# Optimization experiments

Measured on AMD Instinct MI355X. Metric: run time of the kernel, lower is better.

## Reference

```python
import jax, jax.numpy as jnp
import numpy as np
import math

B, H, N, D = 2, 16, 2048, 64

def setup_inputs() -> dict:
    key = jax.random.key(0)
    kq, kk, kv, kb = jax.random.split(key, 4)
    return {
        "query": jax.random.normal(kq, (B, H, N, D), dtype=jnp.float32),
        "key": jax.random.normal(kk, (B, H, N, D), dtype=jnp.float32),
        "value": jax.random.normal(kv, (B, H, N, D), dtype=jnp.float32),
        "relative_position_bias": jax.random.normal(kb, (H, N, N), dtype=jnp.float32),
    }

def reference(query, key, value, relative_position_bias):
    d = query.shape[-1]
    # scores: [B,H,N,N]
    attn = jnp.einsum("bhnd,bhmd->bhnm", query, key) / jnp.sqrt(jnp.asarray(d, query.dtype))
    attn = attn + relative_position_bias[None]  # broadcast over batch
    attn = jax.nn.softmax(attn, axis=-1)
    # dropout p=0.0 -> identity
    output = jnp.einsum("bhnm,bhmd->bhnd", attn, value)
    return (output, attn)
```

## Files before the change

kernel.cpp:

```cpp
#include <hip/hip_runtime.h>
#include <cstdint>

#define BN 2
#define HN 16
#define NN 2048
#define DD 64
#define KT 64
#define NT (NN / KT)
#define LDP 72
#define LDF 68

typedef __attribute__((ext_vector_type(8))) short short8;
typedef __attribute__((ext_vector_type(8))) unsigned short ushort8;
typedef __attribute__((ext_vector_type(4))) float float4v;

static __device__ __forceinline__ unsigned short f2bf(float f){
    uint32_t u = __builtin_bit_cast(uint32_t, f);
    u += 0x7FFFu + ((u >> 16) & 1u);
    return (unsigned short)(u >> 16);
}

static __device__ __forceinline__ float4v mfma_bf16(short8 a, short8 b, float4v c){
    return __builtin_amdgcn_mfma_f32_16x16x32_bf16(a, b, c, 0, 0, 0);
}

static __device__ __forceinline__ void barrier_lds(){
    asm volatile("s_waitcnt lgkmcnt(0)" ::: "memory");
    __builtin_amdgcn_s_barrier();
    asm volatile("" ::: "memory");
}

__launch_bounds__(256, 4)
__global__ void attn_fused_kernel(const float* __restrict__ Q,
                                  const float* __restrict__ K,
                                  const float* __restrict__ V,
                                  const float* __restrict__ Bias,
                                  float* __restrict__ Out){
    __shared__ unsigned short Kb[KT][LDP];
    __shared__ unsigned short Vt[DD][LDP];
    __shared__ float Pb[4][16][LDF];

    const int bid = blockIdx.x;
    const int b   = bid & 1;
    const int t2  = bid >> 1;
    const int rt  = t2 & 31;
    const int h   = t2 >> 5;

    const int tid = threadIdx.x;
    const int l   = tid & 63;
    const int w   = tid >> 6;
    const int lg  = l >> 4;
    const int ll  = l & 15;
    const int vc  = ll * 4;

    const int qw = rt * 64 + w * 16;
    const size_t bh = (size_t)(b * HN + h);
    const float* Qg = Q + (bh * NN + qw) * DD;
    const float* Kg = K + bh * NN * DD;
    const float* Vg = V + bh * NN * DD;
    const float* BgV = Bias + (size_t)h * NN * NN + (size_t)(qw + lg) * NN + vc;

    const int sr = tid >> 2;
    const int sc = (tid & 3) << 4;

    short8 qf[2];
    {
        const float* qrow = Qg + (size_t)ll * DD + lg * 8;
        #pragma unroll
        for(int ks = 0; ks < 2; ++ks){
            float4v f0 = *(const float4v*)(qrow + ks * 32);
            float4v f1 = *(const float4v*)(qrow + ks * 32 + 4);
            short8 s;
            s[0]=(short)f2bf(f0[0]); s[1]=(short)f2bf(f0[1]);
            s[2]=(short)f2bf(f0[2]); s[3]=(short)f2bf(f0[3]);
            s[4]=(short)f2bf(f1[0]); s[5]=(short)f2bf(f1[1]);
            s[6]=(short)f2bf(f1[2]); s[7]=(short)f2bf(f1[3]);
            qf[ks] = s;
        }
    }

    float lsum[4];
    #pragma unroll
    for(int r = 0; r < 4; ++r) lsum[r] = 0.f;

    float4v kreg[4], bv[4];
    {
        const float* src = Kg + (size_t)sr * DD + sc;
        #pragma unroll
        for(int i = 0; i < 4; ++i) kreg[i] = *(const float4v*)(src + i * 4);
        #pragma unroll
        for(int it = 0; it < 4; ++it)
            bv[it] = *(const float4v*)(BgV + (size_t)(it * 4) * NN);
    }

    for(int ct = 0; ct < NT; ++ct){
        barrier_lds();
        {
            unsigned short tmp[16];
            #pragma unroll
            for(int i = 0; i < 4; ++i)
                #pragma unroll
                for(int j = 0; j < 4; ++j)
                    tmp[i*4+j] = f2bf(kreg[i][j]);
            *(ushort8*)&Kb[sr][sc]     = *(ushort8*)&tmp[0];
            *(ushort8*)&Kb[sr][sc + 8] = *(ushort8*)&tmp[8];
        }
        if(ct + 1 < NT){
            const float* src = Kg + (size_t)((ct+1)*KT + sr) * DD + sc;
            #pragma unroll
            for(int i = 0; i < 4; ++i) kreg[i] = *(const float4v*)(src + i * 4);
        }
        barrier_lds();

        #pragma unroll
        for(int it = 0; it < 4; ++it)
            *(float4v*)&Pb[w][it*4 + lg][vc] = bv[it];
        if(ct + 1 < NT){
            #pragma unroll
            for(int it = 0; it < 4; ++it)
                bv[it] = *(const float4v*)(BgV + (size_t)(it * 4) * NN + (ct+1)*KT);
        }

        float4v acc[4];
        #pragma unroll
        for(int sub = 0; sub < 4; ++sub) acc[sub] = (float4v){0.f,0.f,0.f,0.f};
        __builtin_amdgcn_s_setprio(1);
        #pragma unroll
        for(int sub = 0; sub < 4; ++sub){
            short8 b0 = *(const short8*)&Kb[sub*16 + ll][lg*8];
            short8 b1 = *(const short8*)&Kb[sub*16 + ll][32 + lg*8];
            acc[sub] = mfma_bf16(qf[0], b0, acc[sub]);
            acc[sub] = mfma_bf16(qf[1], b1, acc[sub]);
        }
        __builtin_amdgcn_s_setprio(0);

        float e[16];
        #pragma unroll
        for(int sub = 0; sub < 4; ++sub)
            #pragma unroll
            for(int r = 0; r < 4; ++r)
                e[sub*4+r] = __expf(acc[sub][r] * 0.125f + Pb[w][lg*4+r][sub*16+ll]);

        #pragma unroll
        for(int r = 0; r < 4; ++r){
            float ps = (e[r] + e[4+r]) + (e[8+r] + e[12+r]);
            #pragma unroll
            for(int d = 1; d < 16; d <<= 1) ps += __shfl_xor(ps, d);
            lsum[r] += ps;
        }
    }

    float rl[4];
    #pragma unroll
    for(int r = 0; r < 4; ++r) rl[r] = 1.0f / lsum[r];

    float4v oacc[4];
    #pragma unroll
    for(int ds = 0; ds < 4; ++ds) oacc[ds] = (float4v){0.f,0.f,0.f,0.f};

    float* attnW = Out + (size_t)BN*HN*NN*DD
                 + (bh * NN + qw + lg) * (size_t)NN + vc;

    float4v vreg[4];
    {
        const float* ks = Kg + (size_t)sr * DD + sc;
        const float* vs = Vg + (size_t)sr * DD + sc;
        #pragma unroll
        for(int i = 0; i < 4; ++i){
            kreg[i] = *(const float4v*)(ks + i * 4);
            vreg[i] = *(const float4v*)(vs + i * 4);
        }
        #pragma unroll
        for(int it = 0; it < 4; ++it)
            bv[it] = *(const float4v*)(BgV + (size_t)(it * 4) * NN);
    }

    for(int ct = 0; ct < NT; ++ct){
        barrier_lds();
        {
            unsigned short tmp[16];
            #pragma unroll
            for(int i = 0; i < 4; ++i)
                #pragma unroll
                for(int j = 0; j < 4; ++j)
                    tmp[i*4+j] = f2bf(kreg[i][j]);
            *(ushort8*)&Kb[sr][sc]     = *(ushort8*)&tmp[0];
            *(ushort8*)&Kb[sr][sc + 8] = *(ushort8*)&tmp[8];
            #pragma unroll
            for(int i = 0; i < 4; ++i)
                #pragma unroll
                for(int j = 0; j < 4; ++j){
                    const int d = sc + i*4 + j;
                    Vt[d][sr ^ (((d >> 4) & 3) << 4)] = f2bf(vreg[i][j]);
                }
        }
        if(ct + 1 < NT){
            const float* ks = Kg + (size_t)((ct+1)*KT + sr) * DD + sc;
            const float* vs = Vg + (size_t)((ct+1)*KT + sr) * DD + sc;
            #pragma unroll
            for(int i = 0; i < 4; ++i){
                kreg[i] = *(const float4v*)(ks + i * 4);
                vreg[i] = *(const float4v*)(vs + i * 4);
            }
        }
        barrier_lds();

        #pragma unroll
        for(int it = 0; it < 4; ++it)
            *(float4v*)&Pb[w][it*4 + lg][vc] = bv[it];
        if(ct + 1 < NT){
            #pragma unroll
            for(int it = 0; it < 4; ++it)
                bv[it] = *(const float4v*)(BgV + (size_t)(it * 4) * NN + (ct+1)*KT);
        }

        float4v acc[4];
        #pragma unroll
        for(int sub = 0; sub < 4; ++sub) acc[sub] = (float4v){0.f,0.f,0.f,0.f};
        __builtin_amdgcn_s_setprio(1);
        #pragma unroll
        for(int sub = 0; sub < 4; ++sub){
            short8 b0 = *(const short8*)&Kb[sub*16 + ll][lg*8];
            short8 b1 = *(const short8*)&Kb[sub*16 + ll][32 + lg*8];
            acc[sub] = mfma_bf16(qf[0], b0, acc[sub]);
            acc[sub] = mfma_bf16(qf[1], b1, acc[sub]);
        }
        __builtin_amdgcn_s_setprio(0);

        #pragma unroll
        for(int sub = 0; sub < 4; ++sub)
            #pragma unroll
            for(int r = 0; r < 4; ++r){
                float sv = acc[sub][r] * 0.125f + Pb[w][lg*4+r][sub*16+ll];
                Pb[w][lg*4+r][sub*16+ll] = __expf(sv) * rl[r];
            }

        short8 pf0, pf1;
        {
            float4v p0 = *(const float4v*)&Pb[w][ll][lg*8];
            float4v p1 = *(const float4v*)&Pb[w][ll][lg*8 + 4];
            float4v p2 = *(const float4v*)&Pb[w][ll][32 + lg*8];
            float4v p3 = *(const float4v*)&Pb[w][ll][32 + lg*8 + 4];
            #pragma unroll
            for(int j = 0; j < 4; ++j){
                pf0[j]   = (short)f2bf(p0[j]);
                pf0[4+j] = (short)f2bf(p1[j]);
                pf1[j]   = (short)f2bf(p2[j]);
                pf1[4+j] = (short)f2bf(p3[j]);
            }
        }

        #pragma unroll
        for(int it = 0; it < 4; ++it){
            float4v pv = *(const float4v*)&Pb[w][it*4 + lg][vc];
            *(float4v*)(attnW + (size_t)(it*4) * NN + ct*KT) = pv;
        }

        __builtin_amdgcn_s_setprio(1);
        #pragma unroll
        for(int ds = 0; ds < 4; ++ds){
            short8 v0 = *(const short8*)&Vt[ds*16 + ll][(lg*8) ^ (ds<<4)];
            short8 v1 = *(const short8*)&Vt[ds*16 + ll][(32 + lg*8) ^ (ds<<4)];
            oacc[ds] = mfma_bf16(pf0, v0, oacc[ds]);
            oacc[ds] = mfma_bf16(pf1, v1, oacc[ds]);
        }
        __builtin_amdgcn_s_setprio(0);
    }

    float* outG = Out + (bh * NN + qw) * (size_t)DD;
    #pragma unroll
    for(int ds = 0; ds < 4; ++ds)
        #pragma unroll
        for(int r = 0; r < 4; ++r)
            outG[(size_t)(lg*4 + r) * DD + ds*16 + ll] = oacc[ds][r];
}

extern "C" void kernel_launch(void* const* d_in, const int* in_sizes, int n_in,
                              void* d_out, int out_size, void* d_ws, size_t ws_size,
                              hipStream_t stream) {
    const float* q    = (const float*)d_in[0];
    const float* k    = (const float*)d_in[1];
    const float* v    = (const float*)d_in[2];
    const float* bias = (const float*)d_in[3];
    float* out = (float*)d_out;

    dim3 grid(BN * HN * (NN / 64));
    dim3 block(256);
    hipLaunchKernelGGL(attn_fused_kernel, grid, block, 0, stream, q, k, v, bias, out);
}
```

Baseline: 331.0 us.

## Swap MFMA operand order to get transposed score tiles and drop fp32 LDS staging

Swaps the A/B operands of the QK^T and PV MFMAs so each lane holds four consecutive key columns of one query row. Bias can then be loaded straight into registers matching the accumulator layout, and the attention probabilities written to global memory as float4 without the fp32 LDS round-trip. The row-sum reduction shrinks to two cross-lane shuffles after the loop, and P is repacked to bf16 through a small packed LDS buffer for the PV MFMA. Output stores also become vectorized. The cost is extra registers for the double-buffered bias.

```diff
diff --git a/kernel.cpp b/kernel.cpp
--- a/kernel.cpp
+++ b/kernel.cpp
@@ -8,11 +8,12 @@
 #define KT 64
 #define NT (NN / KT)
 #define LDP 72
-#define LDF 68
 
 typedef __attribute__((ext_vector_type(8))) short short8;
 typedef __attribute__((ext_vector_type(8))) unsigned short ushort8;
 typedef __attribute__((ext_vector_type(4))) float float4v;
+typedef __attribute__((ext_vector_type(2))) uint32_t uint2v;
+typedef __attribute__((ext_vector_type(4))) uint32_t uint4v;
 
 static __device__ __forceinline__ unsigned short f2bf(float f){
     uint32_t u = __builtin_bit_cast(uint32_t, f);
@@ -38,7 +39,7 @@
                                   float* __restrict__ Out){
     __shared__ unsigned short Kb[KT][LDP];
     __shared__ unsigned short Vt[DD][LDP];
-    __shared__ float Pb[4][16][LDF];
+    __shared__ __align__(16) uint32_t Pe[4][4][16][12];
 
     const int bid = blockIdx.x;
     const int b   = bid & 1;
@@ -51,14 +52,13 @@
     const int w   = tid >> 6;
     const int lg  = l >> 4;
     const int ll  = l & 15;
-    const int vc  = ll * 4;
 
     const int qw = rt * 64 + w * 16;
     const size_t bh = (size_t)(b * HN + h);
     const float* Qg = Q + (bh * NN + qw) * DD;
     const float* Kg = K + bh * NN * DD;
     const float* Vg = V + bh * NN * DD;
-    const float* BgV = Bias + (size_t)h * NN * NN + (size_t)(qw + lg) * NN + vc;
+    const float* BgA = Bias + (size_t)h * NN * NN + (size_t)(qw + ll) * NN + lg * 4;
 
     const int sr = tid >> 2;
     const int sc = (tid & 3) << 4;
@@ -79,9 +79,7 @@
         }
     }
 
-    float lsum[4];
-    #pragma unroll
-    for(int r = 0; r < 4; ++r) lsum[r] = 0.f;
+    float lsum = 0.f;
 
     float4v kreg[4], bv[4];
     {
@@ -89,8 +87,8 @@
         #pragma unroll
         for(int i = 0; i < 4; ++i) kreg[i] = *(const float4v*)(src + i * 4);
         #pragma unroll
-        for(int it = 0; it < 4; ++it)
-            bv[it] = *(const float4v*)(BgV + (size_t)(it * 4) * NN);
+        for(int sub = 0; sub < 4; ++sub)
+            bv[sub] = *(const float4v*)(BgA + sub * 16);
     }
 
     for(int ct = 0; ct < NT; ++ct){
@@ -112,13 +110,11 @@
         }
         barrier_lds();
 
-        #pragma unroll
-        for(int it = 0; it < 4; ++it)
-            *(float4v*)&Pb[w][it*4 + lg][vc] = bv[it];
-        if(ct + 1 < NT){
-            #pragma unroll
-            for(int it = 0; it < 4; ++it)
-                bv[it] = *(const float4v*)(BgV + (size_t)(it * 4) * NN + (ct+1)*KT);
+        float4v bvN[4];
+        if(ct + 1 < NT){
+            #pragma unroll
+            for(int sub = 0; sub < 4; ++sub)
+                bvN[sub] = *(const float4v*)(BgA + (ct+1)*KT + sub * 16);
         }
 
         float4v acc[4];
@@ -127,39 +123,35 @@
         __builtin_amdgcn_s_setprio(1);
         #pragma unroll
         for(int sub = 0; sub < 4; ++sub){
-            short8 b0 = *(const short8*)&Kb[sub*16 + ll][lg*8];
-            short8 b1 = *(const short8*)&Kb[sub*16 + ll][32 + lg*8];
-            acc[sub] = mfma_bf16(qf[0], b0, acc[sub]);
-            acc[sub] = mfma_bf16(qf[1], b1, acc[sub]);
+            short8 k0 = *(const short8*)&Kb[sub*16 + ll][lg*8];
+            short8 k1 = *(const short8*)&Kb[sub*16 + ll][32 + lg*8];
+            acc[sub] = mfma_bf16(k0, qf[0], acc[sub]);
+            acc[sub] = mfma_bf16(k1, qf[1], acc[sub]);
         }
         __builtin_amdgcn_s_setprio(0);
 
-        float e[16];
         #pragma unroll
         for(int sub = 0; sub < 4; ++sub)
             #pragma unroll
             for(int r = 0; r < 4; ++r)
-                e[sub*4+r] = __expf(acc[sub][r] * 0.125f + Pb[w][lg*4+r][sub*16+ll]);
-
-        #pragma unroll
-        for(int r = 0; r < 4; ++r){
-            float ps = (e[r] + e[4+r]) + (e[8+r] + e[12+r]);
-            #pragma unroll
-            for(int d = 1; d < 16; d <<= 1) ps += __shfl_xor(ps, d);
-            lsum[r] += ps;
-        }
-    }
-
-    float rl[4];
-    #pragma unroll
-    for(int r = 0; r < 4; ++r) rl[r] = 1.0f / lsum[r];
+                lsum += __expf(acc[sub][r] * 0.125f + bv[sub][r]);
+
+        if(ct + 1 < NT){
+            #pragma unroll
+            for(int sub = 0; sub < 4; ++sub) bv[sub] = bvN[sub];
+        }
+    }
+
+    lsum += __shfl_xor(lsum, 16);
+    lsum += __shfl_xor(lsum, 32);
+    const float rl = 1.0f / lsum;
 
     float4v oacc[4];
     #pragma unroll
     for(int ds = 0; ds < 4; ++ds) oacc[ds] = (float4v){0.f,0.f,0.f,0.f};
 
-    float* attnW = Out + (size_t)BN*HN*NN*DD
-                 + (bh * NN + qw + lg) * (size_t)NN + vc;
+    float* attnA = Out + (size_t)BN*HN*NN*DD
+                 + (bh * NN + qw + ll) * (size_t)NN + lg * 4;
 
     float4v vreg[4];
     {
@@ -171,8 +163,8 @@
             vreg[i] = *(const float4v*)(vs + i * 4);
         }
         #pragma unroll
-        for(int it = 0; it < 4; ++it)
-            bv[it] = *(const float4v*)(BgV + (size_t)(it * 4) * NN);
+        for(int sub = 0; sub < 4; ++sub)
+            bv[sub] = *(const float4v*)(BgA + sub * 16);
     }
 
     for(int ct = 0; ct < NT; ++ct){
@@ -205,13 +197,11 @@
         }
         barrier_lds();
 
-        #pragma unroll
-        for(int it = 0; it < 4; ++it)
-            *(float4v*)&Pb[w][it*4 + lg][vc] = bv[it];
-        if(ct + 1 < NT){
-            #pragma unroll
-            for(int it = 0; it < 4; ++it)
-                bv[it] = *(const float4v*)(BgV + (size_t)(it * 4) * NN + (ct+1)*KT);
+        float4v bvN[4];
+        if(ct + 1 < NT){
+            #pragma unroll
+            for(int sub = 0; sub < 4; ++sub)
+                bvN[sub] = *(const float4v*)(BgA + (ct+1)*KT + sub * 16);
         }
 
         float4v acc[4];
@@ -220,40 +210,38 @@
         __builtin_amdgcn_s_setprio(1);
         #pragma unroll
         for(int sub = 0; sub < 4; ++sub){
-            short8 b0 = *(const short8*)&Kb[sub*16 + ll][lg*8];
-            short8 b1 = *(const short8*)&Kb[sub*16 + ll][32 + lg*8];
-            acc[sub] = mfma_bf16(qf[0], b0, acc[sub]);
-            acc[sub] = mfma_bf16(qf[1], b1, acc[sub]);
+            short8 k0 = *(const short8*)&Kb[sub*16 + ll][lg*8];
+            short8 k1 = *(const short8*)&Kb[sub*16 + ll][32 + lg*8];
+            acc[sub] = mfma_bf16(k0, qf[0], acc[sub]);
+            acc[sub] = mfma_bf16(k1, qf[1], acc[sub]);
         }
         __builtin_amdgcn_s_setprio(0);
 
-        #pragma unroll
-        for(int sub = 0; sub < 4; ++sub)
-            #pragma unroll
-            for(int r = 0; r < 4; ++r){
-                float sv = acc[sub][r] * 0.125f + Pb[w][lg*4+r][sub*16+ll];
-                Pb[w][lg*4+r][sub*16+ll] = __expf(sv) * rl[r];
-            }
-
-        short8 pf0, pf1;
-        {
-            float4v p0 = *(const float4v*)&Pb[w][ll][lg*8];
-            float4v p1 = *(const float4v*)&Pb[w][ll][lg*8 + 4];
-            float4v p2 = *(const float4v*)&Pb[w][ll][32 + lg*8];
-            float4v p3 = *(const float4v*)&Pb[w][ll][32 + lg*8 + 4];
-            #pragma unroll
-            for(int j = 0; j < 4; ++j){
-                pf0[j]   = (short)f2bf(p0[j]);
-                pf0[4+j] = (short)f2bf(p1[j]);
-                pf1[j]   = (short)f2bf(p2[j]);
-                pf1[4+j] = (short)f2bf(p3[j]);
-            }
-        }
-
-        #pragma unroll
-        for(int it = 0; it < 4; ++it){
-            float4v pv = *(const float4v*)&Pb[w][it*4 + lg][vc];
-            *(float4v*)(attnW + (size_t)(it*4) * NN + ct*KT) = pv;
+        float4v p4[4];
+        #pragma unroll
+        for(int sub = 0; sub < 4; ++sub)
+            #pragma unroll
+            for(int r = 0; r < 4; ++r)
+                p4[sub][r] = __expf(acc[sub][r] * 0.125f + bv[sub][r]) * rl;
+
+        #pragma unroll
+        for(int sub = 0; sub < 4; ++sub)
+            *(float4v*)(attnA + ct*KT + sub*16) = p4[sub];
+
+        uint32_t pk[8];
+        #pragma unroll
+        for(int sub = 0; sub < 4; ++sub){
+            pk[2*sub]   = (uint32_t)f2bf(p4[sub][0]) | ((uint32_t)f2bf(p4[sub][1]) << 16);
+            pk[2*sub+1] = (uint32_t)f2bf(p4[sub][2]) | ((uint32_t)f2bf(p4[sub][3]) << 16);
+        }
+        #pragma unroll
+        for(int s = 0; s < 4; ++s)
+            *(uint2v*)&Pe[w][s][ll][lg*2] = (uint2v){pk[2*s], pk[2*s+1]};
+        short8 pb[2];
+        #pragma unroll
+        for(int kb = 0; kb < 2; ++kb){
+            uint4v u = *(const uint4v*)&Pe[w][kb*2 + (lg>>1)][ll][(lg&1)*4];
+            pb[kb] = __builtin_bit_cast(short8, u);
         }
 
         __builtin_amdgcn_s_setprio(1);
@@ -261,18 +249,21 @@
         for(int ds = 0; ds < 4; ++ds){
             short8 v0 = *(const short8*)&Vt[ds*16 + ll][(lg*8) ^ (ds<<4)];
             short8 v1 = *(const short8*)&Vt[ds*16 + ll][(32 + lg*8) ^ (ds<<4)];
-            oacc[ds] = mfma_bf16(pf0, v0, oacc[ds]);
-            oacc[ds] = mfma_bf16(pf1, v1, oacc[ds]);
+            oacc[ds] = mfma_bf16(v0, pb[0], oacc[ds]);
+            oacc[ds] = mfma_bf16(v1, pb[1], oacc[ds]);
         }
         __builtin_amdgcn_s_setprio(0);
+
+        if(ct + 1 < NT){
+            #pragma unroll
+            for(int sub = 0; sub < 4; ++sub) bv[sub] = bvN[sub];
+        }
     }
 
     float* outG = Out + (bh * NN + qw) * (size_t)DD;
     #pragma unroll
     for(int ds = 0; ds < 4; ++ds)
-        #pragma unroll
-        for(int r = 0; r < 4; ++r)
-            outG[(size_t)(lg*4 + r) * DD + ds*16 + ll] = oacc[ds][r];
+        *(float4v*)(outG + (size_t)ll * DD + ds*16 + lg*4) = oacc[ds];
 }
 
 extern "C" void kernel_launch(void* const* d_in, const int* in_sizes, int n_in,
```

After: 387.7 us. +17.1%, slower.
